# Kernel optimization log

Measured on AMD Instinct MI355X. Metric: run time of the kernel, lower is better.

Reference implementation:

```python
import jax, jax.numpy as jnp
import numpy as np
import math

N_HEAD = 4
NORM_GROUPS = 32
EPS = 1e-5


def setup_inputs() -> dict:
    key = jax.random.key(0)
    ks = jax.random.split(key, 6)
    C = 256
    x = jax.random.normal(ks[0], (2, C, 64, 64), dtype=jnp.float32)
    gn_w = jnp.ones((C,), dtype=jnp.float32)
    gn_b = jnp.zeros((C,), dtype=jnp.float32)
    s = 1.0 / math.sqrt(C)
    wq = jax.random.normal(ks[1], (C, C), dtype=jnp.float32) * s
    wk = jax.random.normal(ks[2], (C, C), dtype=jnp.float32) * s
    wv = jax.random.normal(ks[3], (C, C), dtype=jnp.float32) * s
    wo = jax.random.normal(ks[4], (C, C), dtype=jnp.float32) * s
    bo = jnp.zeros((C,), dtype=jnp.float32)
    return {"x": x, "gn_w": gn_w, "gn_b": gn_b, "wq": wq, "wk": wk,
            "wv": wv, "wo": wo, "bo": bo}


def group_norm(x, w, b):
    bsz, c, h, wd = x.shape
    xg = x.reshape(bsz, NORM_GROUPS, c // NORM_GROUPS, h, wd)
    mu = jnp.mean(xg, axis=(2, 3, 4), keepdims=True)
    var = jnp.mean(jnp.square(xg - mu), axis=(2, 3, 4), keepdims=True)
    xn = ((xg - mu) * jax.lax.rsqrt(var + EPS)).reshape(bsz, c, h, wd)
    return xn * w[None, :, None, None] + b[None, :, None, None]


def conv1x1(x, w):
    # w: (out_ch, in_ch) applied pointwise
    return jnp.einsum('bchw,oc->bohw', x, w)


def reference(x, gn_w, gn_b, wq, wk, wv, wo, bo):
    bsz, c, h, w = x.shape
    hd = c // N_HEAD
    norm = group_norm(x, gn_w, gn_b)
    q = conv1x1(norm, wq).reshape(bsz, N_HEAD, hd, h, w)
    k = conv1x1(norm, wk).reshape(bsz, N_HEAD, hd, h, w)
    v = conv1x1(norm, wv).reshape(bsz, N_HEAD, hd, h, w)
    # scores over full spatial positions; NOTE: scaled by sqrt(channel), as in source
    scores = jnp.einsum('bnchw,bncxy->bnhwxy', q, k) / jnp.sqrt(jnp.float32(c))
    probs = jax.nn.softmax(scores.reshape(bsz, N_HEAD, h, w, h * w), axis=-1)
    probs = probs.reshape(bsz, N_HEAD, h, w, h, w)
    out = jnp.einsum('bnhwxy,bncxy->bnchw', probs, v).reshape(bsz, c, h, w)
    out = conv1x1(out, wo) + bo[None, :, None, None]
    return out + x
```

## Files before the change

kernel.cpp:

```cpp
#include <hip/hip_runtime.h>

typedef float f32x4 __attribute__((ext_vector_type(4)));
typedef float f32x16 __attribute__((ext_vector_type(16)));
typedef short bf16x8 __attribute__((ext_vector_type(8)));
typedef unsigned short u16;
typedef unsigned int u32;
typedef unsigned int u32x2 __attribute__((ext_vector_type(2)));

#define MFMA(a, b, c) __builtin_amdgcn_mfma_f32_16x16x32_bf16((a), (b), (c), 0, 0, 0)
#define MFMA32(a, b, c) __builtin_amdgcn_mfma_f32_32x32x16_bf16((a), (b), (c), 0, 0, 0)

static __device__ __forceinline__ u16 f2bf(float f) {
    union { float f; u32 u; } v; v.f = f;
    u32 r = v.u + 0x7FFFu + ((v.u >> 16) & 1u);
    return (u16)(r >> 16);
}

static __device__ __forceinline__ u32 pkbf(float a, float b) {
    u32 ua = __float_as_uint(a) + 0x8000u;
    u32 ub = __float_as_uint(b) + 0x8000u;
    return __builtin_amdgcn_perm(ub, ua, 0x07060302);
}

static __device__ __forceinline__ void gll16(const u16* g, u16* l) {
    __builtin_amdgcn_global_load_lds(
        (const __attribute__((address_space(1))) u32*)(const void*)g,
        (__attribute__((address_space(3))) u32*)(void*)l, 16, 0, 0);
}

#define BAR_VM() do { \
    asm volatile("s_waitcnt vmcnt(0)" ::: "memory"); \
    __builtin_amdgcn_s_barrier(); \
    asm volatile("" ::: "memory"); \
} while (0)

__global__ __launch_bounds__(256) void prep_kernel(
    const float* __restrict__ wq, const float* __restrict__ wk,
    const float* __restrict__ wv, const float* __restrict__ wo,
    const float* __restrict__ x, u16* __restrict__ Wbf,
    float2* __restrict__ part) {
    int blk = blockIdx.x;
    int t = threadIdx.x;
    if (blk < 256) {
        int base = (blk * 256 + t) * 4;
        int p = base >> 16;
        int off = base & 65535;
        const float* W = (p == 0) ? wq : ((p == 1) ? wk : ((p == 2) ? wv : wo));
        float sc = (p == 0) ? 0.09014009048f : 1.0f;
        float4 v = *(const float4*)(W + off);
        uint2 pk;
        pk.x = pkbf(v.x * sc, v.y * sc);
        pk.y = pkbf(v.z * sc, v.w * sc);
        *(uint2*)(Wbf + base) = pk;
        return;
    }
    int sblk = blk - 256;
    int bg = sblk >> 2, quarter = sblk & 3;
    const float* xp = x + (size_t)bg * 32768 + quarter * 8192;

    float s = 0.f, ss = 0.f;
#pragma unroll
    for (int rep = 0; rep < 8; ++rep) {
        float4 v = *(const float4*)(xp + t * 4 + rep * 1024);
        s += v.x + v.y + v.z + v.w;
        ss += v.x * v.x + v.y * v.y + v.z * v.z + v.w * v.w;
    }
    for (int off = 1; off < 64; off <<= 1) {
        s += __shfl_xor(s, off);
        ss += __shfl_xor(ss, off);
    }
    __shared__ float red[8];
    int lane = t & 63, w = t >> 6;
    if (lane == 0) { red[w] = s; red[4 + w] = ss; }
    __syncthreads();
    if (t == 0) {
        part[sblk] = make_float2(red[0] + red[1] + red[2] + red[3],
                                 red[4] + red[5] + red[6] + red[7]);
    }
}

__global__ __launch_bounds__(256) void qkv_gemm(
    const float* __restrict__ x, const float* __restrict__ gw,
    const float* __restrict__ gb, const float2* __restrict__ part,
    const u16* __restrict__ Wbf,
    u16* __restrict__ Q, u16* __restrict__ K, u16* __restrict__ V) {
    int b = blockIdx.y & 1;
    int p = blockIdx.y >> 1;
    const u16* W = Wbf + p * 65536;
    int m0 = (blockIdx.x & 1) * 128;
    int n0 = (blockIdx.x >> 1) * 64;

    __shared__ u16 a_s[128 * 40];
    __shared__ u16 b_s[64 * 40];
    __shared__ float wgt_s[256], bia_s[256];

    int t = threadIdx.x;
    int lane = t & 63, wave = t >> 6;
    int wm = wave & 1, wn = wave >> 1;
    int r = lane & 15, qd = lane >> 4;

    {
        int c = t;
        int g = c >> 3;
        float s = 0.f, ss = 0.f;
#pragma unroll
        for (int q = 0; q < 4; ++q) {
            float2 pp = part[(b * 32 + g) * 4 + q];
            s += pp.x; ss += pp.y;
        }
        float mu = s * (1.f / 32768.f);
        float var = ss * (1.f / 32768.f) - mu * mu;
        float rstd = rsqrtf(var + 1e-5f);
        float wg = gw[c] * rstd;
        wgt_s[c] = wg;
        bia_s[c] = gb[c] - mu * wg;
    }
    __syncthreads();

    f32x4 acc[4][2];
#pragma unroll
    for (int i = 0; i < 4; ++i)
#pragma unroll
        for (int j = 0; j < 2; ++j) acc[i][j] = (f32x4){0.f, 0.f, 0.f, 0.f};

    int srow = t >> 1;
    int scp = (t & 1) * 16;
    int bn = t & 63;
    int bw = t >> 6;
    int bswz = ((bn >> 3) & 3) ^ (((bn >> 5) & 1) << 1);
    int bgp = ((bw ^ bswz) << 3);

    for (int kk = 0; kk < 256; kk += 32) {
        __syncthreads();
        {
            const u16* src = W + (m0 + srow) * 256 + kk + scp;
            *(uint4*)(a_s + srow * 40 + scp) = *(const uint4*)(src);
            *(uint4*)(a_s + srow * 40 + scp + 8) = *(const uint4*)(src + 8);
        }
        {
            const float* xcol = x + (size_t)(b * 256 + kk + bw * 8) * 4096 + n0 + bn;
            float xv[8];
#pragma unroll
            for (int j = 0; j < 8; ++j) xv[j] = xcol[(size_t)j * 4096];
#pragma unroll
            for (int j = 0; j < 8; ++j) {
                int c = kk + bw * 8 + j;
                b_s[bn * 40 + bgp + j] = f2bf(xv[j] * wgt_s[c] + bia_s[c]);
            }
        }
        __syncthreads();

        bf16x8 af[4], bf[2];
#pragma unroll
        for (int mt = 0; mt < 4; ++mt)
            af[mt] = *(const bf16x8*)(a_s + (wm * 64 + mt * 16 + r) * 40 + qd * 8);
#pragma unroll
        for (int nt = 0; nt < 2; ++nt) {
            int row = wn * 32 + nt * 16 + r;
            int rswz = ((row >> 3) & 3) ^ (((row >> 5) & 1) << 1);
            bf[nt] = *(const bf16x8*)(b_s + row * 40 + ((qd ^ rswz) << 3));
        }
        if (p == 2) {
#pragma unroll
            for (int mt = 0; mt < 4; ++mt)
#pragma unroll
                for (int nt = 0; nt < 2; ++nt)
                    acc[mt][nt] = MFMA(bf[nt], af[mt], acc[mt][nt]);
        } else {
#pragma unroll
            for (int mt = 0; mt < 4; ++mt)
#pragma unroll
                for (int nt = 0; nt < 2; ++nt)
                    acc[mt][nt] = MFMA(af[mt], bf[nt], acc[mt][nt]);
        }
    }

    if (p < 2) {
        u16* dst = (p == 0) ? Q : K;
#pragma unroll
        for (int mt = 0; mt < 4; ++mt) {
#pragma unroll
            for (int nt = 0; nt < 2; ++nt) {
                int o0 = m0 + wm * 64 + mt * 16 + qd * 4;
                int s = n0 + wn * 32 + nt * 16 + r;
                int h = o0 >> 6, d0 = o0 & 63;
                uint2 pk;
                pk.x = pkbf(acc[mt][nt][0], acc[mt][nt][1]);
                pk.y = pkbf(acc[mt][nt][2], acc[mt][nt][3]);
                *(uint2*)(dst + ((size_t)((b * 4 + h) * 4096 + s)) * 64 + d0) = pk;
            }
        }
    } else {
#pragma unroll
        for (int mt = 0; mt < 4; ++mt) {
#pragma unroll
            for (int nt = 0; nt < 2; ++nt) {
                int o = m0 + wm * 64 + mt * 16 + r;
                int h = o >> 6, d = o & 63;
                int sb = n0 + wn * 32 + nt * 16 + qd * 4;
                uint2 pk;
                pk.x = pkbf(acc[mt][nt][0], acc[mt][nt][1]);
                pk.y = pkbf(acc[mt][nt][2], acc[mt][nt][3]);
                *(uint2*)(V + ((size_t)((b * 4 + h) * 64 + d)) * 4096 + sb) = pk;
            }
        }
    }
}

template <int QT>
__global__ __launch_bounds__(256, QT == 1 ? 4 : 2) void attn_kernel(
    const u16* __restrict__ Q, const u16* __restrict__ K,
    const u16* __restrict__ V, u16* __restrict__ Opart,
    float* __restrict__ Lpart, int nk32) {
    int bh = blockIdx.x & 7, sp = blockIdx.x >> 3;
    int qb = blockIdx.y;
    int t = threadIdx.x, lane = t & 63, w = t >> 6;
    int qn = lane & 31, h = lane >> 5;

    const size_t bhoff = (size_t)bh * 4096 * 64;
    int q0 = (qb * 4 + w) * (32 * QT);
    int kbase = sp * nk32 * 32;

    __shared__ u16 smem[16384];

    bf16x8 qf[QT][4];
#pragma unroll
    for (int qt = 0; qt < QT; ++qt)
#pragma unroll
        for (int c = 0; c < 4; ++c)
            qf[qt][c] = *(const bf16x8*)(Q + bhoff +
                (size_t)(q0 + qt * 32 + qn) * 64 + c * 16 + h * 8);

    f32x16 oacc[2][QT];
#pragma unroll
    for (int dt = 0; dt < 2; ++dt)
#pragma unroll
        for (int qt = 0; qt < QT; ++qt)
#pragma unroll
            for (int i = 0; i < 16; ++i) oacc[dt][qt][i] = 0.f;
    float lacc[QT];
#pragma unroll
    for (int qt = 0; qt < QT; ++qt) lacc[qt] = 0.f;

    const u16* Kp = K + bhoff;
    const u16* Vp = V + bhoff;

    int gs = (lane & 7) ^ (lane >> 3);
    int rbase = (w & 1) * 32 + (lane >> 3);

    auto fill = [&](int bufsel, int kp) {
        u16* ld = smem + bufsel * 8192 + w * 2048;
        if (w < 2) {
            const u16* s = Kp + (size_t)(kp + rbase) * 64 + gs * 8;
#pragma unroll
            for (int j = 0; j < 4; ++j) gll16(s + j * 512, ld + j * 512);
        } else {
            const u16* s = Vp + (size_t)rbase * 4096 + kp + gs * 8;
#pragma unroll
            for (int j = 0; j < 4; ++j) gll16(s + j * 32768, ld + j * 512);
        }
    };

    int sw = qn & 7;
    auto step = [&](const u16* buf, int j) {
        bf16x8 kf[4], vf[2][2];
        int kr = j * 32 + qn;
#pragma unroll
        for (int c = 0; c < 4; ++c)
            kf[c] = *(const bf16x8*)(buf + kr * 64 + (((c * 2 + h) ^ sw) << 3));
#pragma unroll
        for (int dt = 0; dt < 2; ++dt) {
            int d = dt * 32 + qn;
#pragma unroll
            for (int kc = 0; kc < 2; ++kc) {
                int g = j * 4 + kc * 2 + h;
                vf[dt][kc] = *(const bf16x8*)(buf + 4096 + d * 64 + ((g ^ sw) << 3));
            }
        }
#pragma unroll
        for (int qt = 0; qt < QT; ++qt) {
            f32x16 s;
#pragma unroll
            for (int i = 0; i < 16; ++i) s[i] = 0.f;
            __builtin_amdgcn_s_setprio(1);
#pragma unroll
            for (int c = 0; c < 4; ++c) s = MFMA32(kf[c], qf[qt][c], s);
            __builtin_amdgcn_s_setprio(0);

            float e[16];
#pragma unroll
            for (int i = 0; i < 16; ++i)
                e[i] = __builtin_amdgcn_exp2f(s[i]);
            float t0 = (e[0] + e[1]) + (e[2] + e[3]);
            float t1 = (e[4] + e[5]) + (e[6] + e[7]);
            float t2 = (e[8] + e[9]) + (e[10] + e[11]);
            float t3 = (e[12] + e[13]) + (e[14] + e[15]);
            lacc[qt] += (t0 + t1) + (t2 + t3);

            u32 p[8];
#pragma unroll
            for (int i = 0; i < 8; ++i) p[i] = pkbf(e[2 * i], e[2 * i + 1]);

            u32x2 r0 = __builtin_amdgcn_permlane32_swap(p[0], p[2], false, false);
            u32x2 r1 = __builtin_amdgcn_permlane32_swap(p[1], p[3], false, false);
            u32x2 r2 = __builtin_amdgcn_permlane32_swap(p[4], p[6], false, false);
            u32x2 r3 = __builtin_amdgcn_permlane32_swap(p[5], p[7], false, false);
            uint4 pau = {r0[0], r1[0], r0[1], r1[1]};
            uint4 pbu = {r2[0], r3[0], r2[1], r3[1]};
            bf16x8 pA = *(const bf16x8*)&pau;
            bf16x8 pB = *(const bf16x8*)&pbu;

            __builtin_amdgcn_s_setprio(1);
#pragma unroll
            for (int dt = 0; dt < 2; ++dt) {
                oacc[dt][qt] = MFMA32(vf[dt][0], pA, oacc[dt][qt]);
                oacc[dt][qt] = MFMA32(vf[dt][1], pB, oacc[dt][qt]);
            }
            __builtin_amdgcn_s_setprio(0);
        }
    };

    int npair = nk32 >> 1;
    fill(0, kbase);
    if (npair > 1) fill(1, kbase + 64);
    BAR_VM();

    for (int i = 0; i < npair; ++i) {
        const u16* cur = smem + (i & 1) * 8192;
        step(cur, 0);
        step(cur, 1);
        BAR_VM();
        if (i + 2 < npair) fill(i & 1, kbase + (i + 2) * 64);
    }

    float lfull[QT];
#pragma unroll
    for (int qt = 0; qt < QT; ++qt)
        lfull[qt] = lacc[qt] + __shfl_xor(lacc[qt], 32);

    u16* my = smem + w * (32 * 72);
    size_t obase = ((size_t)sp * 8 + bh) * 4096 + q0;
#pragma unroll
    for (int qt = 0; qt < QT; ++qt) {
#pragma unroll
        for (int dt = 0; dt < 2; ++dt) {
#pragma unroll
            for (int g = 0; g < 4; ++g) {
                int d0 = g * 8 + h * 4 + dt * 32;
                uint2 pk;
                pk.x = pkbf(oacc[dt][qt][4 * g], oacc[dt][qt][4 * g + 1]);
                pk.y = pkbf(oacc[dt][qt][4 * g + 2], oacc[dt][qt][4 * g + 3]);
                *(uint2*)(my + qn * 72 + d0) = pk;
            }
        }
#pragma unroll
        for (int rr = 0; rr < 4; ++rr) {
            int row = rr * 8 + (lane >> 3), ch = lane & 7;
            uint4 v = *(const uint4*)(my + row * 72 + ch * 8);
            *(uint4*)(Opart + (obase + qt * 32 + row) * 64 + ch * 8) = v;
        }
    }
    if (h == 0) {
#pragma unroll
        for (int qt = 0; qt < QT; ++qt)
            Lpart[obase + qt * 32 + qn] = lfull[qt];
    }
}

__global__ __launch_bounds__(256) void attn_combine(
    const u16* __restrict__ Opart, const float* __restrict__ Lpart,
    u16* __restrict__ attnT, int nsplit) {
    int t = threadIdx.x;
    int gr = blockIdx.x * 64 + (t >> 2);
    int d0 = (t & 3) * 16;

    float l = 0.f;
    for (int s = 0; s < nsplit; ++s) l += Lpart[(size_t)s * 32768 + gr];
    float inv = 1.f / l;

    float acc[16];
#pragma unroll
    for (int i = 0; i < 16; ++i) acc[i] = 0.f;
    for (int s = 0; s < nsplit; ++s) {
        const u16* p = Opart + ((size_t)s * 32768 + gr) * 64 + d0;
        uint4 a = *(const uint4*)(p);
        uint4 bq = *(const uint4*)(p + 8);
        const u32* ap = (const u32*)&a;
        const u32* bp = (const u32*)&bq;
#pragma unroll
        for (int j = 0; j < 4; ++j) {
            acc[2 * j]     += __uint_as_float(ap[j] << 16);
            acc[2 * j + 1] += __uint_as_float(ap[j] & 0xFFFF0000u);
            acc[8 + 2 * j]     += __uint_as_float(bp[j] << 16);
            acc[8 + 2 * j + 1] += __uint_as_float(bp[j] & 0xFFFF0000u);
        }
    }
    u32 pk[8];
#pragma unroll
    for (int j = 0; j < 8; ++j)
        pk[j] = pkbf(acc[2 * j] * inv, acc[2 * j + 1] * inv);

    int bh = gr >> 12, q = gr & 4095;
    int b = bh >> 2, hh = bh & 3;
    u16* dst = attnT + ((size_t)(b * 4096 + q)) * 256 + hh * 64 + d0;
    *(uint4*)(dst) = make_uint4(pk[0], pk[1], pk[2], pk[3]);
    *(uint4*)(dst + 8) = make_uint4(pk[4], pk[5], pk[6], pk[7]);
}

__global__ __launch_bounds__(256) void out_gemm(
    const u16* __restrict__ attnT, const u16* __restrict__ W3,
    const float* __restrict__ bo, const float* __restrict__ x,
    float* __restrict__ out) {
    int b = blockIdx.y;
    int m0 = (blockIdx.x & 3) * 64;
    int n0 = (blockIdx.x >> 2) * 64;

    __shared__ u16 a_s[64 * 40];
    __shared__ u16 b_s[64 * 40];

    int t = threadIdx.x;
    int lane = t & 63, wave = t >> 6;
    int wm = wave & 1, wn = wave >> 1;
    int r = lane & 15, qd = lane >> 4;

    const u16* Bsrc = attnT + (size_t)b * 4096 * 256;

    f32x4 acc[2][2];
#pragma unroll
    for (int i = 0; i < 2; ++i)
#pragma unroll
        for (int j = 0; j < 2; ++j) acc[i][j] = (f32x4){0.f, 0.f, 0.f, 0.f};

    int u = t & 127;
    int srow = u >> 1;
    int scp = (u & 1) * 16;

    for (int kk = 0; kk < 256; kk += 32) {
        __syncthreads();
        if (t < 128) {
            const u16* src = W3 + (m0 + srow) * 256 + kk + scp;
            *(uint4*)(a_s + srow * 40 + scp) = *(const uint4*)(src);
            *(uint4*)(a_s + srow * 40 + scp + 8) = *(const uint4*)(src + 8);
        } else {
            const u16* src = Bsrc + (size_t)(n0 + srow) * 256 + kk + scp;
            *(uint4*)(b_s + srow * 40 + scp) = *(const uint4*)(src);
            *(uint4*)(b_s + srow * 40 + scp + 8) = *(const uint4*)(src + 8);
        }
        __syncthreads();

        bf16x8 af[2], bf[2];
#pragma unroll
        for (int mt = 0; mt < 2; ++mt)
            af[mt] = *(const bf16x8*)(a_s + (wm * 32 + mt * 16 + r) * 40 + qd * 8);
#pragma unroll
        for (int nt = 0; nt < 2; ++nt)
            bf[nt] = *(const bf16x8*)(b_s + (wn * 32 + nt * 16 + r) * 40 + qd * 8);
#pragma unroll
        for (int mt = 0; mt < 2; ++mt)
#pragma unroll
            for (int nt = 0; nt < 2; ++nt)
                acc[mt][nt] = MFMA(af[mt], bf[nt], acc[mt][nt]);
    }

#pragma unroll
    for (int mt = 0; mt < 2; ++mt) {
#pragma unroll
        for (int nt = 0; nt < 2; ++nt) {
#pragma unroll
            for (int j = 0; j < 4; ++j) {
                int o = m0 + wm * 32 + mt * 16 + qd * 4 + j;
                int s = n0 + wn * 32 + nt * 16 + r;
                size_t idx = (size_t)(b * 256 + o) * 4096 + s;
                out[idx] = acc[mt][nt][j] + bo[o] + x[idx];
            }
        }
    }
}

extern "C" void kernel_launch(void* const* d_in, const int* in_sizes, int n_in,
                              void* d_out, int out_size, void* d_ws, size_t ws_size,
                              hipStream_t stream) {
    const float* x = (const float*)d_in[0];
    const float* gn_w = (const float*)d_in[1];
    const float* gn_b = (const float*)d_in[2];
    const float* wq = (const float*)d_in[3];
    const float* wk = (const float*)d_in[4];
    const float* wv = (const float*)d_in[5];
    const float* wo = (const float*)d_in[6];
    const float* bo = (const float*)d_in[7];
    float* out = (float*)d_out;

    char* ws = (char*)d_ws;
    u16* attnT = (u16*)(ws);
    u16* Q     = (u16*)(ws + (4u << 20));
    u16* Kp    = (u16*)(ws + (8u << 20));
    u16* Vp    = (u16*)(ws + (12u << 20));
    u16* Wbf   = (u16*)(ws + (16u << 20));
    float2* part = (float2*)(ws + (16u << 20) + 524288);

    size_t opart_off = (size_t)17 << 20;
    size_t osplit = 8ull * 4096 * 64 * 2;
    int nsplit = (ws_size >= opart_off + 4 * osplit + 4ull * 32768 * 4 + 4096) ? 4 : 2;
    u16* Opart = (u16*)(ws + opart_off);
    float* Lpart = (float*)(ws + opart_off + (size_t)nsplit * osplit);

    prep_kernel<<<512, 256, 0, stream>>>(wq, wk, wv, wo, x, Wbf, part);
    qkv_gemm<<<dim3(128, 6), 256, 0, stream>>>(x, gn_w, gn_b, part, Wbf, Q, Kp, Vp);
    attn_kernel<1><<<dim3(8 * nsplit, 32), 256, 0, stream>>>(
        Q, Kp, Vp, Opart, Lpart, 128 / nsplit);
    attn_combine<<<512, 256, 0, stream>>>(Opart, Lpart, attnT, nsplit);
    out_gemm<<<dim3(256, 2), 256, 0, stream>>>(attnT, Wbf + 3 * 65536, bo, x, out);
}
```

Baseline: 142.9 us.

## Fuse split-attention combine into output projection GEMM

Removes the separate attn_combine kernel. The output GEMM now reads the per-split partial outputs and log-sum denominators directly, sums and normalizes them while staging its B tile, and packs the result to bf16 in shared memory. The N tile shrinks from 64 to 32 and the grid doubles, so there are more blocks and less per-wave MFMA work. This saves one launch and the attnT round trip through memory, but each W3 tile is now loaded by twice as many blocks.

```diff
diff --git a/kernel.cpp b/kernel.cpp
--- a/kernel.cpp
+++ b/kernel.cpp
@@ -32,6 +32,11 @@
     asm volatile("s_waitcnt vmcnt(0)" ::: "memory"); \
     __builtin_amdgcn_s_barrier(); \
     asm volatile("" ::: "memory"); \
+} while (0)
+
+#define BAR_LGKM() do { \
+    asm volatile("s_waitcnt lgkmcnt(0)" ::: "memory"); \
+    __builtin_amdgcn_s_barrier(); \
 } while (0)
 
 __global__ __launch_bounds__(256) void prep_kernel(
@@ -367,112 +372,82 @@
     }
 }
 
-__global__ __launch_bounds__(256) void attn_combine(
+__global__ __launch_bounds__(256) void out_gemm(
     const u16* __restrict__ Opart, const float* __restrict__ Lpart,
-    u16* __restrict__ attnT, int nsplit) {
-    int t = threadIdx.x;
-    int gr = blockIdx.x * 64 + (t >> 2);
-    int d0 = (t & 3) * 16;
-
-    float l = 0.f;
-    for (int s = 0; s < nsplit; ++s) l += Lpart[(size_t)s * 32768 + gr];
-    float inv = 1.f / l;
-
-    float acc[16];
-#pragma unroll
-    for (int i = 0; i < 16; ++i) acc[i] = 0.f;
-    for (int s = 0; s < nsplit; ++s) {
-        const u16* p = Opart + ((size_t)s * 32768 + gr) * 64 + d0;
-        uint4 a = *(const uint4*)(p);
-        uint4 bq = *(const uint4*)(p + 8);
-        const u32* ap = (const u32*)&a;
-        const u32* bp = (const u32*)&bq;
-#pragma unroll
-        for (int j = 0; j < 4; ++j) {
-            acc[2 * j]     += __uint_as_float(ap[j] << 16);
-            acc[2 * j + 1] += __uint_as_float(ap[j] & 0xFFFF0000u);
-            acc[8 + 2 * j]     += __uint_as_float(bp[j] << 16);
-            acc[8 + 2 * j + 1] += __uint_as_float(bp[j] & 0xFFFF0000u);
-        }
-    }
-    u32 pk[8];
-#pragma unroll
-    for (int j = 0; j < 8; ++j)
-        pk[j] = pkbf(acc[2 * j] * inv, acc[2 * j + 1] * inv);
-
-    int bh = gr >> 12, q = gr & 4095;
-    int b = bh >> 2, hh = bh & 3;
-    u16* dst = attnT + ((size_t)(b * 4096 + q)) * 256 + hh * 64 + d0;
-    *(uint4*)(dst) = make_uint4(pk[0], pk[1], pk[2], pk[3]);
-    *(uint4*)(dst + 8) = make_uint4(pk[4], pk[5], pk[6], pk[7]);
-}
-
-__global__ __launch_bounds__(256) void out_gemm(
-    const u16* __restrict__ attnT, const u16* __restrict__ W3,
-    const float* __restrict__ bo, const float* __restrict__ x,
-    float* __restrict__ out) {
+    const u16* __restrict__ W3, const float* __restrict__ bo,
+    const float* __restrict__ x, float* __restrict__ out, int nsplit) {
     int b = blockIdx.y;
     int m0 = (blockIdx.x & 3) * 64;
-    int n0 = (blockIdx.x >> 2) * 64;
+    int n0 = (blockIdx.x >> 2) * 32;
 
     __shared__ u16 a_s[64 * 40];
-    __shared__ u16 b_s[64 * 40];
+    __shared__ u16 b_s[32 * 40];
+    __shared__ float linv_s[4][32];
 
     int t = threadIdx.x;
     int lane = t & 63, wave = t >> 6;
     int wm = wave & 1, wn = wave >> 1;
     int r = lane & 15, qd = lane >> 4;
 
-    const u16* Bsrc = attnT + (size_t)b * 4096 * 256;
-
-    f32x4 acc[2][2];
-#pragma unroll
-    for (int i = 0; i < 2; ++i)
-#pragma unroll
-        for (int j = 0; j < 2; ++j) acc[i][j] = (f32x4){0.f, 0.f, 0.f, 0.f};
-
-    int u = t & 127;
-    int srow = u >> 1;
-    int scp = (u & 1) * 16;
+    if (t < 128) {
+        int hh = t >> 5, row = t & 31;
+        size_t gi = (size_t)(b * 4 + hh) * 4096 + n0 + row;
+        float l = 0.f;
+        for (int s = 0; s < nsplit; ++s) l += Lpart[(size_t)s * 32768 + gi];
+        linv_s[hh][row] = 1.f / l;
+    }
+
+    f32x4 acc[2];
+    acc[0] = (f32x4){0.f, 0.f, 0.f, 0.f};
+    acc[1] = (f32x4){0.f, 0.f, 0.f, 0.f};
+
+    int arow = t >> 2, acp = (t & 3) * 8;
+    int brow = t >> 3, bcp = (t & 7) * 4;
+    __syncthreads();
 
     for (int kk = 0; kk < 256; kk += 32) {
-        __syncthreads();
-        if (t < 128) {
-            const u16* src = W3 + (m0 + srow) * 256 + kk + scp;
-            *(uint4*)(a_s + srow * 40 + scp) = *(const uint4*)(src);
-            *(uint4*)(a_s + srow * 40 + scp + 8) = *(const uint4*)(src + 8);
-        } else {
-            const u16* src = Bsrc + (size_t)(n0 + srow) * 256 + kk + scp;
-            *(uint4*)(b_s + srow * 40 + scp) = *(const uint4*)(src);
-            *(uint4*)(b_s + srow * 40 + scp + 8) = *(const uint4*)(src + 8);
-        }
-        __syncthreads();
-
-        bf16x8 af[2], bf[2];
+        {
+            const u16* src = W3 + (m0 + arow) * 256 + kk + acp;
+            *(uint4*)(a_s + arow * 40 + acp) = *(const uint4*)(src);
+        }
+        {
+            int hh = kk >> 6, dk = kk & 63;
+            size_t base = ((size_t)(b * 4 + hh) * 4096 + n0 + brow) * 64 + dk + bcp;
+            float a0 = 0.f, a1 = 0.f, a2 = 0.f, a3 = 0.f;
+            for (int s = 0; s < nsplit; ++s) {
+                uint2 v = *(const uint2*)(Opart + (size_t)s * 2097152 + base);
+                a0 += __uint_as_float(v.x << 16);
+                a1 += __uint_as_float(v.x & 0xFFFF0000u);
+                a2 += __uint_as_float(v.y << 16);
+                a3 += __uint_as_float(v.y & 0xFFFF0000u);
+            }
+            float li = linv_s[hh][brow];
+            uint2 pk;
+            pk.x = pkbf(a0 * li, a1 * li);
+            pk.y = pkbf(a2 * li, a3 * li);
+            *(uint2*)(b_s + brow * 40 + bcp) = pk;
+        }
+        BAR_LGKM();
+
+        bf16x8 af[2], bf;
 #pragma unroll
         for (int mt = 0; mt < 2; ++mt)
             af[mt] = *(const bf16x8*)(a_s + (wm * 32 + mt * 16 + r) * 40 + qd * 8);
-#pragma unroll
-        for (int nt = 0; nt < 2; ++nt)
-            bf[nt] = *(const bf16x8*)(b_s + (wn * 32 + nt * 16 + r) * 40 + qd * 8);
+        bf = *(const bf16x8*)(b_s + (wn * 16 + r) * 40 + qd * 8);
 #pragma unroll
         for (int mt = 0; mt < 2; ++mt)
-#pragma unroll
-            for (int nt = 0; nt < 2; ++nt)
-                acc[mt][nt] = MFMA(af[mt], bf[nt], acc[mt][nt]);
+            acc[mt] = MFMA(af[mt], bf, acc[mt]);
+        BAR_LGKM();
     }
 
 #pragma unroll
     for (int mt = 0; mt < 2; ++mt) {
 #pragma unroll
-        for (int nt = 0; nt < 2; ++nt) {
-#pragma unroll
-            for (int j = 0; j < 4; ++j) {
-                int o = m0 + wm * 32 + mt * 16 + qd * 4 + j;
-                int s = n0 + wn * 32 + nt * 16 + r;
-                size_t idx = (size_t)(b * 256 + o) * 4096 + s;
-                out[idx] = acc[mt][nt][j] + bo[o] + x[idx];
-            }
+        for (int j = 0; j < 4; ++j) {
+            int o = m0 + wm * 32 + mt * 16 + qd * 4 + j;
+            int s = n0 + wn * 16 + r;
+            size_t idx = (size_t)(b * 256 + o) * 4096 + s;
+            out[idx] = acc[mt][j] + bo[o] + x[idx];
         }
     }
 }
@@ -491,7 +466,6 @@
     float* out = (float*)d_out;
 
     char* ws = (char*)d_ws;
-    u16* attnT = (u16*)(ws);
     u16* Q     = (u16*)(ws + (4u << 20));
     u16* Kp    = (u16*)(ws + (8u << 20));
     u16* Vp    = (u16*)(ws + (12u << 20));
@@ -508,6 +482,6 @@
     qkv_gemm<<<dim3(128, 6), 256, 0, stream>>>(x, gn_w, gn_b, part, Wbf, Q, Kp, Vp);
     attn_kernel<1><<<dim3(8 * nsplit, 32), 256, 0, stream>>>(
         Q, Kp, Vp, Opart, Lpart, 128 / nsplit);
-    attn_combine<<<512, 256, 0, stream>>>(Opart, Lpart, attnT, nsplit);
-    out_gemm<<<dim3(256, 2), 256, 0, stream>>>(attnT, Wbf + 3 * 65536, bo, x, out);
-}
+    out_gemm<<<dim3(512, 2), 256, 0, stream>>>(
+        Opart, Lpart, Wbf + 3 * 65536, bo, x, out, nsplit);
+}
```

Result: slower. 158.1 us (+10.7%).

## Double-buffer LDS tiles with register prefetch in QKV and output GEMMs

Applied to the files above, without the earlier changes.

Both the QKV projection GEMM and the output projection GEMM now keep two LDS tile buffers. The next K-slice is loaded from global memory into registers while MFMAs run on the current buffer, and is written to the other buffer afterwards. This removes one of the two barriers per K step and hides global load latency behind compute. In exchange it doubles LDS use, adds register pressure, and leaves only 8 iterations of K to overlap.

```diff
diff --git a/kernel.cpp b/kernel.cpp
--- a/kernel.cpp
+++ b/kernel.cpp
@@ -32,6 +32,11 @@
     asm volatile("s_waitcnt vmcnt(0)" ::: "memory"); \
     __builtin_amdgcn_s_barrier(); \
     asm volatile("" ::: "memory"); \
+} while (0)
+
+#define BAR_LGKM() do { \
+    asm volatile("s_waitcnt lgkmcnt(0)" ::: "memory"); \
+    __builtin_amdgcn_s_barrier(); \
 } while (0)
 
 __global__ __launch_bounds__(256) void prep_kernel(
@@ -90,8 +95,8 @@
     int m0 = (blockIdx.x & 1) * 128;
     int n0 = (blockIdx.x >> 1) * 64;
 
-    __shared__ u16 a_s[128 * 40];
-    __shared__ u16 b_s[64 * 40];
+    __shared__ u16 a_s[2][128 * 40];
+    __shared__ u16 b_s[2][64 * 40];
     __shared__ float wgt_s[256], bia_s[256];
 
     int t = threadIdx.x;
@@ -130,35 +135,44 @@
     int bswz = ((bn >> 3) & 3) ^ (((bn >> 5) & 1) << 1);
     int bgp = ((bw ^ bswz) << 3);
 
-    for (int kk = 0; kk < 256; kk += 32) {
-        __syncthreads();
-        {
-            const u16* src = W + (m0 + srow) * 256 + kk + scp;
-            *(uint4*)(a_s + srow * 40 + scp) = *(const uint4*)(src);
-            *(uint4*)(a_s + srow * 40 + scp + 8) = *(const uint4*)(src + 8);
-        }
-        {
-            const float* xcol = x + (size_t)(b * 256 + kk + bw * 8) * 4096 + n0 + bn;
-            float xv[8];
-#pragma unroll
-            for (int j = 0; j < 8; ++j) xv[j] = xcol[(size_t)j * 4096];
-#pragma unroll
-            for (int j = 0; j < 8; ++j) {
-                int c = kk + bw * 8 + j;
-                b_s[bn * 40 + bgp + j] = f2bf(xv[j] * wgt_s[c] + bia_s[c]);
-            }
-        }
-        __syncthreads();
+    uint4 pa0, pa1;
+    float pxv[8];
+    auto load_regs = [&](int kk) {
+        const u16* src = W + (m0 + srow) * 256 + kk + scp;
+        pa0 = *(const uint4*)(src);
+        pa1 = *(const uint4*)(src + 8);
+        const float* xcol = x + (size_t)(b * 256 + kk + bw * 8) * 4096 + n0 + bn;
+#pragma unroll
+        for (int j = 0; j < 8; ++j) pxv[j] = xcol[(size_t)j * 4096];
+    };
+    auto write_buf = [&](int bsel, int kk) {
+        *(uint4*)(a_s[bsel] + srow * 40 + scp) = pa0;
+        *(uint4*)(a_s[bsel] + srow * 40 + scp + 8) = pa1;
+#pragma unroll
+        for (int j = 0; j < 8; ++j) {
+            int c = kk + bw * 8 + j;
+            b_s[bsel][bn * 40 + bgp + j] = f2bf(pxv[j] * wgt_s[c] + bia_s[c]);
+        }
+    };
+
+    load_regs(0);
+    write_buf(0, 0);
+    BAR_LGKM();
+
+    for (int it = 0; it < 8; ++it) {
+        int cur = it & 1;
+        bool more = (it + 1) < 8;
+        if (more) load_regs((it + 1) * 32);
 
         bf16x8 af[4], bf[2];
 #pragma unroll
         for (int mt = 0; mt < 4; ++mt)
-            af[mt] = *(const bf16x8*)(a_s + (wm * 64 + mt * 16 + r) * 40 + qd * 8);
+            af[mt] = *(const bf16x8*)(a_s[cur] + (wm * 64 + mt * 16 + r) * 40 + qd * 8);
 #pragma unroll
         for (int nt = 0; nt < 2; ++nt) {
             int row = wn * 32 + nt * 16 + r;
             int rswz = ((row >> 3) & 3) ^ (((row >> 5) & 1) << 1);
-            bf[nt] = *(const bf16x8*)(b_s + row * 40 + ((qd ^ rswz) << 3));
+            bf[nt] = *(const bf16x8*)(b_s[cur] + row * 40 + ((qd ^ rswz) << 3));
         }
         if (p == 2) {
 #pragma unroll
@@ -173,6 +187,9 @@
                 for (int nt = 0; nt < 2; ++nt)
                     acc[mt][nt] = MFMA(af[mt], bf[nt], acc[mt][nt]);
         }
+
+        if (more) write_buf(cur ^ 1, (it + 1) * 32);
+        BAR_LGKM();
     }
 
     if (p < 2) {
@@ -415,8 +432,8 @@
     int m0 = (blockIdx.x & 3) * 64;
     int n0 = (blockIdx.x >> 2) * 64;
 
-    __shared__ u16 a_s[64 * 40];
-    __shared__ u16 b_s[64 * 40];
+    __shared__ u16 a_s[2][64 * 40];
+    __shared__ u16 b_s[2][64 * 40];
 
     int t = threadIdx.x;
     int lane = t & 63, wave = t >> 6;
@@ -435,31 +452,45 @@
     int srow = u >> 1;
     int scp = (u & 1) * 16;
 
-    for (int kk = 0; kk < 256; kk += 32) {
-        __syncthreads();
-        if (t < 128) {
-            const u16* src = W3 + (m0 + srow) * 256 + kk + scp;
-            *(uint4*)(a_s + srow * 40 + scp) = *(const uint4*)(src);
-            *(uint4*)(a_s + srow * 40 + scp + 8) = *(const uint4*)(src + 8);
-        } else {
-            const u16* src = Bsrc + (size_t)(n0 + srow) * 256 + kk + scp;
-            *(uint4*)(b_s + srow * 40 + scp) = *(const uint4*)(src);
-            *(uint4*)(b_s + srow * 40 + scp + 8) = *(const uint4*)(src + 8);
-        }
-        __syncthreads();
+    uint4 p0, p1;
+    auto load_regs = [&](int kk) {
+        const u16* src = (t < 128)
+            ? W3 + (m0 + srow) * 256 + kk + scp
+            : Bsrc + (size_t)(n0 + srow) * 256 + kk + scp;
+        p0 = *(const uint4*)(src);
+        p1 = *(const uint4*)(src + 8);
+    };
+    auto write_buf = [&](int bsel) {
+        u16* dst = (t < 128) ? (a_s[bsel] + srow * 40 + scp)
+                             : (b_s[bsel] + srow * 40 + scp);
+        *(uint4*)(dst) = p0;
+        *(uint4*)(dst + 8) = p1;
+    };
+
+    load_regs(0);
+    write_buf(0);
+    BAR_LGKM();
+
+    for (int it = 0; it < 8; ++it) {
+        int cur = it & 1;
+        bool more = (it + 1) < 8;
+        if (more) load_regs((it + 1) * 32);
 
         bf16x8 af[2], bf[2];
 #pragma unroll
         for (int mt = 0; mt < 2; ++mt)
-            af[mt] = *(const bf16x8*)(a_s + (wm * 32 + mt * 16 + r) * 40 + qd * 8);
+            af[mt] = *(const bf16x8*)(a_s[cur] + (wm * 32 + mt * 16 + r) * 40 + qd * 8);
 #pragma unroll
         for (int nt = 0; nt < 2; ++nt)
-            bf[nt] = *(const bf16x8*)(b_s + (wn * 32 + nt * 16 + r) * 40 + qd * 8);
+            bf[nt] = *(const bf16x8*)(b_s[cur] + (wn * 32 + nt * 16 + r) * 40 + qd * 8);
 #pragma unroll
         for (int mt = 0; mt < 2; ++mt)
 #pragma unroll
             for (int nt = 0; nt < 2; ++nt)
                 acc[mt][nt] = MFMA(af[mt], bf[nt], acc[mt][nt]);
+
+        if (more) write_buf(cur ^ 1);
+        BAR_LGKM();
     }
 
 #pragma unroll
```

New measurement: 139.8 us. -2.1%, faster.
